# Kernel optimization log

Measured on AMD Instinct MI355X. Metric: run time of the kernel, lower is better.

The kernel has to match this reference:

```python
import jax, jax.numpy as jnp
import numpy as np

K = 4  # Chebyshev order (layer._k)

def setup_inputs() -> dict:
    key = jax.random.key(0)
    k1, k2, k3, k4 = jax.random.split(key, 4)
    N, din, dout = 4096, 128, 128
    a = jax.random.normal(k1, (N, din), dtype=jnp.float32)            # layer input (only len used)
    r = jax.random.uniform(k2, (N, dout), dtype=jnp.float32)          # upstream relevance (positive)
    # sparse-ish binary directed adjacency, no self loops (avg degree ~16)
    adj = (jax.random.uniform(k3, (N, N)) < (16.0 / N)).astype(jnp.float32)
    adj = adj * (1.0 - jnp.eye(N, dtype=jnp.float32))
    W = jax.random.normal(k4, (dout, K * din), dtype=jnp.float32) * 0.05  # ChebConv linear weight [out, K*in]
    return {"a": a, "r": r, "adj": adj, "W": W}

def _forward(a, r, adj, W):
    N = a.shape[0]
    dW = W.shape[1] // K
    # Wk[k] = W[:, k*dW:(k+1)*dW].T  -> [K, dimY(in), dimJ(out)]; rho = abs
    rhoW = jnp.abs(jnp.stack([W[:, k * dW:(k + 1) * dW].T for k in range(K)]))
    # Laplacian: L = I - D^{-1/2} A D^{-1/2}, degrees clamped at 1 (in-degrees = column sums)
    dinv = jnp.clip(adj.sum(axis=0), 1.0, None) ** -0.5
    D = dinv[:, None] * adj * dinv[None, :]
    L = jnp.eye(N, dtype=adj.dtype) - D
    # Chebyshev polynomials T_0=I, T_1=L, T_k = 2 L T_{k-1} - T_{k-2}  -> [K, N, N]
    Ts = [jnp.eye(N, dtype=L.dtype), L]
    for _ in range(2, K):
        Ts.append(2.0 * (L @ Ts[-1]) - Ts[-2])
    Ak = jnp.stack(Ts[:K])
    # U[i,j,x,y] = sum_k Ak[k,i,x] * rhoW[k,y,j]; never materialized.
    # denom[i,j] = U.sum(dim=(2,3)) = sum_k (sum_x Ak[k,i,x]) * (sum_y rhoW[k,y,j])
    denom = jnp.einsum('ki,kj->ij', Ak.sum(axis=2), rhoW.sum(axis=1))
    c = r / denom
    # out[x,y] = einsum('ijxy,ij->xy', U, c) = sum_k Ak[k].T @ c @ rhoW[k].T
    return jnp.einsum('kix,kyj,ij->xy', Ak, rhoW, c)

def reference(a, r, adj, W):
    return _forward(a, r, adj, W)
```

## Files before the change

### kernel.cpp

```cpp
#include <hip/hip_runtime.h>
#include <cstdint>
#include <cstddef>

#define N_NODES 4096
#define FEAT 128
#define KCH 4
#define NNZ_CAP (1 << 18)
#define TB 512
#define T2CAP 2048
#define RSTRIDE 96

__device__ __forceinline__ int panel_of(int p) {
    return p < 3456 ? (p / 384) : (p < 3776 ? 9 : 10);
}

__global__ __launch_bounds__(256) void k_adj(const float* __restrict__ adj,
                                             int* __restrict__ deg,
                                             int* __restrict__ rdeg,
                                             int* __restrict__ rcolF) {
    int row = (blockIdx.x * 256 + threadIdx.x) >> 6;
    int lane = threadIdx.x & 63;
    const float* rowp = adj + (size_t)row * N_NODES;
    int base = 0;
    for (int it = 0; it < 64; ++it) {
        int x = it * 64 + lane;
        bool nz = rowp[x] != 0.0f;
        unsigned long long m = __ballot(nz);
        if (nz) {
            int idx = base + __popcll(m & ((1ull << lane) - 1ull));
            if (idx < RSTRIDE) rcolF[row * RSTRIDE + idx] = x;
            atomicAdd(&deg[x], 1);
        }
        base += __popcll(m);
    }
    if (lane == 0) rdeg[row] = (base > RSTRIDE) ? RSTRIDE : base;
}

__global__ __launch_bounds__(1024) void k_scan(const int* __restrict__ deg,
                                               float* __restrict__ dinv,
                                               int* __restrict__ colptr,
                                               int* __restrict__ colcur) {
    __shared__ int wsum[16];
    __shared__ int wbase[16];
    int t = threadIdx.x;
    int lane = t & 63, wv = t >> 6;
    int v[4]; int s = 0;
    for (int c = 0; c < 4; ++c) {
        int idx = t * 4 + c;
        int di = deg[idx];
        v[c] = di;
        s += di;
        float dc = fmaxf((float)di, 1.0f);
        dinv[idx] = (float)(1.0 / sqrt((double)dc));
    }
    int sc = s;
    for (int off = 1; off < 64; off <<= 1) {
        int n = __shfl_up(sc, off);
        if (lane >= off) sc += n;
    }
    if (lane == 63) wsum[wv] = sc;
    __syncthreads();
    if (t == 0) {
        int b = 0;
        for (int q2 = 0; q2 < 16; ++q2) { wbase[q2] = b; b += wsum[q2]; }
    }
    __syncthreads();
    int base = wbase[wv] + sc - s;
    for (int c = 0; c < 4; ++c) {
        int idx = t * 4 + c;
        colptr[idx] = base; colcur[idx] = base;
        base += v[c];
    }
    if (t == 1023) colptr[N_NODES] = base;
}

__global__ __launch_bounds__(256) void k_vals(const float* __restrict__ dinv,
                                              const int* __restrict__ rdeg,
                                              const int* __restrict__ rcolF,
                                              float* __restrict__ rlvalF,
                                              int* __restrict__ colcur,
                                              int* __restrict__ col_i,
                                              float* __restrict__ val) {
    int row = (blockIdx.x * 256 + threadIdx.x) >> 6;
    int lane = threadIdx.x & 63;
    int n = rdeg[row];
    float di = dinv[row];
    for (int e = lane; e < n; e += 64) {
        int x = rcolF[row * RSTRIDE + e];
        float dv = di * dinv[x];
        rlvalF[row * RSTRIDE + e] = -dv;
        int ec = atomicAdd(&colcur[x], 1);
        if (ec < NNZ_CAP) { col_i[ec] = row; val[ec] = dv; }
    }
}

__global__ void k_sw(const float* __restrict__ W, float* __restrict__ sW) {
    int tid = blockIdx.x * blockDim.x + threadIdx.x;
    int k = tid >> 7, j = tid & 127;
    float s = 0.f;
    for (int y = 0; y < FEAT; ++y)
        s += fabsf(W[(size_t)j * (KCH * FEAT) + k * FEAT + y]);
    sW[k * FEAT + j] = s;
}

__device__ __forceinline__ float np_pairwise_4096(const float* __restrict__ row,
                                                  float* r256, float* leaf,
                                                  float* bc, int t) {
    if (t < 256) {
        int L = t >> 3, j = t & 7;
        const float* p = row + L * 128 + j;
        float a = p[0];
        #pragma unroll
        for (int q = 1; q < 16; ++q) a += p[8 * q];
        r256[t] = a;
    }
    __syncthreads();
    if (t < 32) {
        const float* rr = r256 + t * 8;
        leaf[t] = ((rr[0] + rr[1]) + (rr[2] + rr[3])) + ((rr[4] + rr[5]) + (rr[6] + rr[7]));
    }
    __syncthreads();
    if (t == 0) {
        float v[32];
        #pragma unroll
        for (int q = 0; q < 32; ++q) v[q] = leaf[q];
        #pragma unroll
        for (int w = 16; w >= 1; w >>= 1)
            #pragma unroll
            for (int q = 0; q < 16; ++q)
                if (q < w) v[q] = v[2 * q] + v[2 * q + 1];
        bc[0] = v[0];
    }
    __syncthreads();
    float res = bc[0];
    __syncthreads();
    return res;
}

__global__ __launch_bounds__(TB) void k_t2(const int* __restrict__ rdeg,
                                           const int* __restrict__ rcolF,
                                           const float* __restrict__ rlvalF,
                                           int2* __restrict__ t2sp,
                                           int* __restrict__ t2cnt,
                                           float* __restrict__ sA) {
    __shared__ float gp[N_NODES];
    __shared__ int   scol[2048];
    __shared__ float sval[2048];
    __shared__ int   pcol[64];
    __shared__ float pLip[64];
    __shared__ int   pbeg[64], plen[64], poff[65];
    __shared__ int   ssplit;
    __shared__ float r256[256], leaf[32], bc[1];
    __shared__ int   wtot[8], wbase[8];
    int t = threadIdx.x;
    int i = blockIdx.x;
    int rp = i * RSTRIDE;
    int ol = rdeg[i];
    int cnt = ol + 1;
    if (cnt > 64) cnt = 64;
    if (t == 0) ssplit = 0;
    __syncthreads();
    if (t < ol && rcolF[rp + t] < i) atomicAdd(&ssplit, 1);
    __syncthreads();
    int split = ssplit;
    if (t < cnt) {
        int col; float lip;
        if (t < split)       { col = rcolF[rp + t];     lip = rlvalF[rp + t]; }
        else if (t == split) { col = i;                 lip = 1.0f; }
        else                 { col = rcolF[rp + t - 1]; lip = rlvalF[rp + t - 1]; }
        pcol[t] = col; pLip[t] = lip;
        pbeg[t] = col * RSTRIDE;
        plen[t] = rdeg[col] + 1;
    }
    float4* gp4 = (float4*)gp;
    const float4 z4 = make_float4(0.f, 0.f, 0.f, 0.f);
    #pragma unroll
    for (int u = 0; u < 2; ++u) gp4[t + u * TB] = z4;
    __syncthreads();
    if (t == 0) {
        int o = 0;
        for (int q = 0; q < cnt; ++q) { poff[q] = o; o += plen[q]; }
        poff[cnt] = o;
    }
    __syncthreads();
    int E = poff[cnt]; if (E > 2048) E = 2048;
    for (int idx = t; idx < E; idx += TB) {
        int lo = 0, hi = cnt - 1;
        while (lo < hi) { int mid = (lo + hi + 1) >> 1; if (poff[mid] <= idx) lo = mid; else hi = mid - 1; }
        int e = idx - poff[lo];
        if (e == plen[lo] - 1) { scol[idx] = pcol[lo]; sval[idx] = 1.0f; }
        else                   { scol[idx] = rcolF[pbeg[lo] + e]; sval[idx] = rlvalF[pbeg[lo] + e]; }
    }
    __syncthreads();
    int q0 = split;
    for (int e = t; e < plen[q0]; e += TB) { int idx = poff[q0] + e; gp[scol[idx]] = sval[idx]; }
    __syncthreads();
    float s1 = np_pairwise_4096(gp, r256, leaf, bc, t);
    for (int e = t; e < plen[q0]; e += TB) gp[scol[poff[q0] + e]] = 0.0f;
    __syncthreads();
    float tot[8];
    #pragma unroll
    for (int u = 0; u < 8; ++u) tot[u] = 0.0f;
    int q = 0;
    while (q < cnt) {
        int pid = panel_of(pcol[q]);
        while (q < cnt && panel_of(pcol[q]) == pid) {
            float lv = pLip[q];
            int o = poff[q], Lq = plen[q];
            for (int e = t; e < Lq; e += TB) {
                int idx = o + e; int x = scol[idx];
                gp[x] = fmaf(lv, sval[idx], gp[x]);
            }
            __syncthreads();
            ++q;
        }
        #pragma unroll
        for (int u2 = 0; u2 < 2; ++u2) {
            int idx = t + u2 * TB;
            float4 b = gp4[idx];
            tot[4 * u2 + 0] = tot[4 * u2 + 0] + b.x;
            tot[4 * u2 + 1] = tot[4 * u2 + 1] + b.y;
            tot[4 * u2 + 2] = tot[4 * u2 + 2] + b.z;
            tot[4 * u2 + 3] = tot[4 * u2 + 3] + b.w;
            gp4[idx] = z4;
        }
        __syncthreads();
    }
    #pragma unroll
    for (int u2 = 0; u2 < 2; ++u2) {
        int xb = 4 * t + 2048 * u2;
        float4 v;
        v.x = 2.0f * tot[4 * u2 + 0] - (xb + 0 == i ? 1.0f : 0.0f);
        v.y = 2.0f * tot[4 * u2 + 1] - (xb + 1 == i ? 1.0f : 0.0f);
        v.z = 2.0f * tot[4 * u2 + 2] - (xb + 2 == i ? 1.0f : 0.0f);
        v.w = 2.0f * tot[4 * u2 + 3] - (xb + 3 == i ? 1.0f : 0.0f);
        gp4[t + u2 * TB] = v;
    }
    __syncthreads();
    float s2 = np_pairwise_4096(gp, r256, leaf, bc, t);
    float4 ea = gp4[2 * t], eb = gp4[2 * t + 1];
    float ev[8] = {ea.x, ea.y, ea.z, ea.w, eb.x, eb.y, eb.z, eb.w};
    int cl = 0;
    #pragma unroll
    for (int u = 0; u < 8; ++u) cl += (ev[u] != 0.0f);
    int lane = t & 63, wv = t >> 6;
    int sc = cl;
    for (int off = 1; off < 64; off <<= 1) {
        int n = __shfl_up(sc, off);
        if (lane >= off) sc += n;
    }
    if (lane == 63) wtot[wv] = sc;
    __syncthreads();
    if (t == 0) {
        int b = 0;
        for (int wq = 0; wq < 8; ++wq) { wbase[wq] = b; b += wtot[wq]; }
        t2cnt[i] = (b > T2CAP) ? T2CAP : b;
    }
    __syncthreads();
    int pos = wbase[wv] + sc - cl;
    int2* dst = t2sp + (size_t)i * T2CAP;
    #pragma unroll
    for (int u = 0; u < 8; ++u) {
        if (ev[u] != 0.0f) {
            if (pos < T2CAP) dst[pos] = make_int2(t * 8 + u, __float_as_int(ev[u]));
            ++pos;
        }
    }
    if (t == 0) {
        sA[0 * N_NODES + i] = 1.0f;
        sA[1 * N_NODES + i] = s1;
        sA[2 * N_NODES + i] = s2;
    }
}

__global__ __launch_bounds__(TB) void k_t3(const int* __restrict__ rdeg,
                                           const int* __restrict__ rcolF,
                                           const float* __restrict__ rlvalF,
                                           const int2* __restrict__ t2sp,
                                           const int* __restrict__ t2cnt,
                                           float* __restrict__ sA) {
    __shared__ float gp[N_NODES];
    __shared__ int   pcol[64];
    __shared__ float pLip[64];
    __shared__ int   pnn[64];
    __shared__ int   ssplit;
    __shared__ float r256[256], leaf[32], bc[1];
    int t = threadIdx.x;
    int i = blockIdx.x;
    int rp = i * RSTRIDE;
    int ol = rdeg[i];
    int cnt = ol + 1;
    if (cnt > 64) cnt = 64;
    if (t == 0) ssplit = 0;
    __syncthreads();
    if (t < ol && rcolF[rp + t] < i) atomicAdd(&ssplit, 1);
    __syncthreads();
    int split = ssplit;
    if (t < cnt) {
        int col; float lip;
        if (t < split)       { col = rcolF[rp + t];     lip = rlvalF[rp + t]; }
        else if (t == split) { col = i;                  lip = 1.0f; }
        else                 { col = rcolF[rp + t - 1];  lip = rlvalF[rp + t - 1]; }
        pcol[t] = col; pLip[t] = lip; pnn[t] = t2cnt[col];
    }
    float4* gp4 = (float4*)gp;
    const float4 z4 = make_float4(0.f, 0.f, 0.f, 0.f);
    #pragma unroll
    for (int u2 = 0; u2 < 2; ++u2) gp4[t + u2 * TB] = z4;
    __syncthreads();
    float tot[8];
    #pragma unroll
    for (int u = 0; u < 8; ++u) tot[u] = 0.0f;
    int2 enb[4] = {make_int2(0, 0), make_int2(0, 0), make_int2(0, 0), make_int2(0, 0)};
    int nn_next = pnn[0];
    {
        const int2* sp = t2sp + (size_t)pcol[0] * T2CAP;
        #pragma unroll
        for (int u = 0; u < 4; ++u) { int e = t + u * TB; if (e < nn_next) enb[u] = sp[e]; }
    }
    int q = 0;
    while (q < cnt) {
        int2 cur[4];
        int nn_c = nn_next;
        #pragma unroll
        for (int u = 0; u < 4; ++u) cur[u] = enb[u];
        if (q + 1 < cnt) {
            nn_next = pnn[q + 1];
            const int2* sp = t2sp + (size_t)pcol[q + 1] * T2CAP;
            #pragma unroll
            for (int u = 0; u < 4; ++u) { int e = t + u * TB; if (e < nn_next) enb[u] = sp[e]; }
        }
        float lv = pLip[q];
        #pragma unroll
        for (int u = 0; u < 4; ++u) {
            int e = t + u * TB;
            if (e < nn_c) gp[cur[u].x] = fmaf(lv, __int_as_float(cur[u].y), gp[cur[u].x]);
        }
        __syncthreads();
        ++q;
        if (q == cnt || panel_of(pcol[q]) != panel_of(pcol[q - 1])) {
            #pragma unroll
            for (int u2 = 0; u2 < 2; ++u2) {
                int idx = t + u2 * TB;
                float4 b = gp4[idx];
                tot[4 * u2 + 0] = tot[4 * u2 + 0] + b.x;
                tot[4 * u2 + 1] = tot[4 * u2 + 1] + b.y;
                tot[4 * u2 + 2] = tot[4 * u2 + 2] + b.z;
                tot[4 * u2 + 3] = tot[4 * u2 + 3] + b.w;
                gp4[idx] = z4;
            }
            __syncthreads();
        }
    }
    #pragma unroll
    for (int u2 = 0; u2 < 2; ++u2) {
        float4 v;
        v.x = 2.0f * tot[4 * u2 + 0];
        v.y = 2.0f * tot[4 * u2 + 1];
        v.z = 2.0f * tot[4 * u2 + 2];
        v.w = 2.0f * tot[4 * u2 + 3];
        gp4[t + u2 * TB] = v;
    }
    __syncthreads();
    for (int e = t; e < ol; e += TB) { int x = rcolF[rp + e]; gp[x] = gp[x] - rlvalF[rp + e]; }
    if (t == 0) gp[i] = gp[i] - 1.0f;
    __syncthreads();
    float s3 = np_pairwise_4096(gp, r256, leaf, bc, t);
    if (t == 0) sA[3 * N_NODES + i] = s3;
}

__global__ __launch_bounds__(256) void k_cm(const float* __restrict__ r,
                                            const float* __restrict__ sA,
                                            const float* __restrict__ sW,
                                            const float* __restrict__ W,
                                            float* __restrict__ M) {
#pragma clang fp contract(off)
    __shared__ float cl[16][FEAT];
    int k = blockIdx.y;
    int ib = blockIdx.x * 16;
    int tx = threadIdx.x;
    int y = tx & 127, half = tx >> 7;
    for (int m = tx; m < 16 * FEAT; m += 256) {
        int i = ib + (m >> 7), j = m & 127;
        float denom = 0.0f;
        #pragma unroll
        for (int k2 = 0; k2 < KCH; ++k2) {
            float p = sA[k2 * N_NODES + i] * sW[k2 * FEAT + j];
            denom = denom + p;
        }
        cl[m >> 7][m & 127] = r[(size_t)i * FEAT + j] / denom;
    }
    __syncthreads();
    float acc[8];
    #pragma unroll
    for (int u = 0; u < 8; ++u) acc[u] = 0.0f;
    for (int j = 0; j < FEAT; ++j) {
        float a = fabsf(W[(size_t)j * (KCH * FEAT) + k * FEAT + y]);
        #pragma unroll
        for (int u = 0; u < 8; ++u) acc[u] += a * cl[half * 8 + u][j];
    }
    #pragma unroll
    for (int u = 0; u < 8; ++u)
        M[(size_t)k * N_NODES * FEAT + (size_t)(ib + half * 8 + u) * FEAT + y] = acc[u];
}

__global__ void k_h1(const int* __restrict__ colptr, const int* __restrict__ col_i,
                     const float* __restrict__ val, const float* __restrict__ M,
                     float* __restrict__ B2) {
    int x = blockIdx.x * 2 + (threadIdx.x >> 7);
    int y = threadIdx.x & 127;
    const float* M2 = M + (size_t)2 * N_NODES * FEAT;
    const float* M3 = M + (size_t)3 * N_NODES * FEAT;
    int e0 = colptr[x], e1 = colptr[x + 1];
    if (e1 > NNZ_CAP) e1 = NNZ_CAP;
    float g = 0.0f;
    for (int e = e0; e < e1; ++e)
        g += val[e] * M3[(size_t)col_i[e] * FEAT + y];
    size_t o = (size_t)x * FEAT + y;
    B2[o] = 2.0f * M2[o] + 4.0f * (M3[o] - g);
}

__global__ void k_h2(const int* __restrict__ colptr, const int* __restrict__ col_i,
                     const float* __restrict__ val, const float* __restrict__ M,
                     const float* __restrict__ B2, float* __restrict__ B3) {
    int x = blockIdx.x * 2 + (threadIdx.x >> 7);
    int y = threadIdx.x & 127;
    const float* M1 = M + (size_t)N_NODES * FEAT;
    const float* M3 = M + (size_t)3 * N_NODES * FEAT;
    int e0 = colptr[x], e1 = colptr[x + 1];
    if (e1 > NNZ_CAP) e1 = NNZ_CAP;
    float g = 0.0f;
    for (int e = e0; e < e1; ++e)
        g += val[e] * B2[(size_t)col_i[e] * FEAT + y];
    size_t o = (size_t)x * FEAT + y;
    B3[o] = (M1[o] - 3.0f * M3[o]) + (B2[o] - g);
}

__global__ void k_h3(const int* __restrict__ colptr, const int* __restrict__ col_i,
                     const float* __restrict__ val, const float* __restrict__ M,
                     const float* __restrict__ B3, float* __restrict__ out) {
    int x = blockIdx.x * 2 + (threadIdx.x >> 7);
    int y = threadIdx.x & 127;
    const float* M0 = M;
    const float* M2 = M + (size_t)2 * N_NODES * FEAT;
    int e0 = colptr[x], e1 = colptr[x + 1];
    if (e1 > NNZ_CAP) e1 = NNZ_CAP;
    float g = 0.0f;
    for (int e = e0; e < e1; ++e)
        g += val[e] * B3[(size_t)col_i[e] * FEAT + y];
    size_t o = (size_t)x * FEAT + y;
    out[o] = (M0[o] - M2[o]) + (B3[o] - g);
}

extern "C" void kernel_launch(void* const* d_in, const int* in_sizes, int n_in,
                              void* d_out, int out_size, void* d_ws, size_t ws_size,
                              hipStream_t stream) {
    const float* r   = (const float*)d_in[1];
    const float* adj = (const float*)d_in[2];
    const float* W   = (const float*)d_in[3];
    float* out = (float*)d_out;

    char* w = (char*)d_ws;
    auto take = [&](size_t bytes) {
        char* p = w;
        w += (bytes + 255) & ~(size_t)255;
        return p;
    };
    int*   deg    = (int*)take((size_t)N_NODES * 4);
    int*   rdeg   = (int*)take((size_t)N_NODES * 4);
    float* dinv   = (float*)take((size_t)N_NODES * 4);
    int*   colcur = (int*)take((size_t)N_NODES * 4);
    int*   colptr = (int*)take((size_t)(N_NODES + 1) * 4);
    int*   col_i  = (int*)take((size_t)NNZ_CAP * 4);
    float* val    = (float*)take((size_t)NNZ_CAP * 4);
    int*   rcolF  = (int*)take((size_t)N_NODES * RSTRIDE * 4);
    float* rlvalF = (float*)take((size_t)N_NODES * RSTRIDE * 4);
    float* sW     = (float*)take((size_t)KCH * FEAT * 4);
    float* sA     = (float*)take((size_t)KCH * N_NODES * 4);
    float* M      = (float*)take((size_t)KCH * N_NODES * FEAT * 4);
    float* B2     = (float*)take((size_t)N_NODES * FEAT * 4);
    float* B3     = (float*)take((size_t)N_NODES * FEAT * 4);
    int*   t2cnt  = (int*)take((size_t)N_NODES * 4);
    int2*  t2sp   = (int2*)take((size_t)N_NODES * T2CAP * 8);

    hipMemsetAsync(deg, 0, (size_t)N_NODES * 4, stream);
    k_adj<<<N_NODES / 4, 256, 0, stream>>>(adj, deg, rdeg, rcolF);
    k_scan<<<1, 1024, 0, stream>>>(deg, dinv, colptr, colcur);
    k_vals<<<N_NODES / 4, 256, 0, stream>>>(dinv, rdeg, rcolF, rlvalF,
                                            colcur, col_i, val);
    k_sw<<<2, 256, 0, stream>>>(W, sW);
    k_t2<<<N_NODES, TB, 0, stream>>>(rdeg, rcolF, rlvalF, t2sp, t2cnt, sA);
    k_t3<<<N_NODES, TB, 0, stream>>>(rdeg, rcolF, rlvalF, t2sp, t2cnt, sA);
    k_cm<<<dim3(N_NODES / 16, KCH), 256, 0, stream>>>(r, sA, sW, W, M);
    k_h1<<<N_NODES / 2, 256, 0, stream>>>(colptr, col_i, val, M, B2);
    k_h2<<<N_NODES / 2, 256, 0, stream>>>(colptr, col_i, val, M, B2, B3);
    k_h3<<<N_NODES / 2, 256, 0, stream>>>(colptr, col_i, val, M, B3, out);
}
```

Baseline: 363.9 us.

## Shrink k_t3 blocks to 256 threads, drop register prefetch, fold k_sw into k_vals

k_t3 now runs 256-thread blocks. The software-pipelined register prefetch of the next T2 row is replaced by a simple strided loop over the current row, with 16 per-thread accumulators instead of 8. The goal is lower register pressure and more resident blocks per CU for the LDS-scatter loop, at the cost of losing the load/compute overlap. The small |W| column-sum kernel is also merged into k_vals as two extra blocks, which saves one kernel launch.

New measurement: 343.4 us. -5.6%, faster.

```diff
diff --git a/kernel.cpp b/kernel.cpp
--- a/kernel.cpp
+++ b/kernel.cpp
@@ -7,6 +7,7 @@
 #define KCH 4
 #define NNZ_CAP (1 << 18)
 #define TB 512
+#define TB3 256
 #define T2CAP 2048
 #define RSTRIDE 96
 
@@ -80,7 +81,18 @@
                                               float* __restrict__ rlvalF,
                                               int* __restrict__ colcur,
                                               int* __restrict__ col_i,
-                                              float* __restrict__ val) {
+                                              float* __restrict__ val,
+                                              const float* __restrict__ W,
+                                              float* __restrict__ sW) {
+    if (blockIdx.x >= N_NODES / 4) {
+        int tid = (blockIdx.x - N_NODES / 4) * 256 + threadIdx.x;
+        int k = tid >> 7, j = tid & 127;
+        float s = 0.f;
+        for (int y = 0; y < FEAT; ++y)
+            s += fabsf(W[(size_t)j * (KCH * FEAT) + k * FEAT + y]);
+        sW[k * FEAT + j] = s;
+        return;
+    }
     int row = (blockIdx.x * 256 + threadIdx.x) >> 6;
     int lane = threadIdx.x & 63;
     int n = rdeg[row];
@@ -92,15 +104,6 @@
         int ec = atomicAdd(&colcur[x], 1);
         if (ec < NNZ_CAP) { col_i[ec] = row; val[ec] = dv; }
     }
-}
-
-__global__ void k_sw(const float* __restrict__ W, float* __restrict__ sW) {
-    int tid = blockIdx.x * blockDim.x + threadIdx.x;
-    int k = tid >> 7, j = tid & 127;
-    float s = 0.f;
-    for (int y = 0; y < FEAT; ++y)
-        s += fabsf(W[(size_t)j * (KCH * FEAT) + k * FEAT + y]);
-    sW[k * FEAT + j] = s;
 }
 
 __device__ __forceinline__ float np_pairwise_4096(const float* __restrict__ row,
@@ -273,12 +276,12 @@
     }
 }
 
-__global__ __launch_bounds__(TB) void k_t3(const int* __restrict__ rdeg,
-                                           const int* __restrict__ rcolF,
-                                           const float* __restrict__ rlvalF,
-                                           const int2* __restrict__ t2sp,
-                                           const int* __restrict__ t2cnt,
-                                           float* __restrict__ sA) {
+__global__ __launch_bounds__(TB3) void k_t3(const int* __restrict__ rdeg,
+                                            const int* __restrict__ rcolF,
+                                            const float* __restrict__ rlvalF,
+                                            const int2* __restrict__ t2sp,
+                                            const int* __restrict__ t2cnt,
+                                            float* __restrict__ sA) {
     __shared__ float gp[N_NODES];
     __shared__ int   pcol[64];
     __shared__ float pLip[64];
@@ -306,42 +309,28 @@
     float4* gp4 = (float4*)gp;
     const float4 z4 = make_float4(0.f, 0.f, 0.f, 0.f);
     #pragma unroll
-    for (int u2 = 0; u2 < 2; ++u2) gp4[t + u2 * TB] = z4;
-    __syncthreads();
-    float tot[8];
-    #pragma unroll
-    for (int u = 0; u < 8; ++u) tot[u] = 0.0f;
-    int2 enb[4] = {make_int2(0, 0), make_int2(0, 0), make_int2(0, 0), make_int2(0, 0)};
-    int nn_next = pnn[0];
-    {
-        const int2* sp = t2sp + (size_t)pcol[0] * T2CAP;
-        #pragma unroll
-        for (int u = 0; u < 4; ++u) { int e = t + u * TB; if (e < nn_next) enb[u] = sp[e]; }
-    }
+    for (int u2 = 0; u2 < 4; ++u2) gp4[t + u2 * TB3] = z4;
+    __syncthreads();
+    float tot[16];
+    #pragma unroll
+    for (int u = 0; u < 16; ++u) tot[u] = 0.0f;
     int q = 0;
     while (q < cnt) {
-        int2 cur[4];
-        int nn_c = nn_next;
-        #pragma unroll
-        for (int u = 0; u < 4; ++u) cur[u] = enb[u];
-        if (q + 1 < cnt) {
-            nn_next = pnn[q + 1];
-            const int2* sp = t2sp + (size_t)pcol[q + 1] * T2CAP;
-            #pragma unroll
-            for (int u = 0; u < 4; ++u) { int e = t + u * TB; if (e < nn_next) enb[u] = sp[e]; }
-        }
-        float lv = pLip[q];
-        #pragma unroll
-        for (int u = 0; u < 4; ++u) {
-            int e = t + u * TB;
-            if (e < nn_c) gp[cur[u].x] = fmaf(lv, __int_as_float(cur[u].y), gp[cur[u].x]);
-        }
-        __syncthreads();
+        {
+            float lv = pLip[q];
+            int nn = pnn[q];
+            const int2* sp = t2sp + (size_t)pcol[q] * T2CAP;
+            for (int e = t; e < nn; e += TB3) {
+                int2 en = sp[e];
+                gp[en.x] = fmaf(lv, __int_as_float(en.y), gp[en.x]);
+            }
+            __syncthreads();
+        }
         ++q;
         if (q == cnt || panel_of(pcol[q]) != panel_of(pcol[q - 1])) {
             #pragma unroll
-            for (int u2 = 0; u2 < 2; ++u2) {
-                int idx = t + u2 * TB;
+            for (int u2 = 0; u2 < 4; ++u2) {
+                int idx = t + u2 * TB3;
                 float4 b = gp4[idx];
                 tot[4 * u2 + 0] = tot[4 * u2 + 0] + b.x;
                 tot[4 * u2 + 1] = tot[4 * u2 + 1] + b.y;
@@ -353,16 +342,16 @@
         }
     }
     #pragma unroll
-    for (int u2 = 0; u2 < 2; ++u2) {
+    for (int u2 = 0; u2 < 4; ++u2) {
         float4 v;
         v.x = 2.0f * tot[4 * u2 + 0];
         v.y = 2.0f * tot[4 * u2 + 1];
         v.z = 2.0f * tot[4 * u2 + 2];
         v.w = 2.0f * tot[4 * u2 + 3];
-        gp4[t + u2 * TB] = v;
-    }
-    __syncthreads();
-    for (int e = t; e < ol; e += TB) { int x = rcolF[rp + e]; gp[x] = gp[x] - rlvalF[rp + e]; }
+        gp4[t + u2 * TB3] = v;
+    }
+    __syncthreads();
+    for (int e = t; e < ol; e += TB3) { int x = rcolF[rp + e]; gp[x] = gp[x] - rlvalF[rp + e]; }
     if (t == 0) gp[i] = gp[i] - 1.0f;
     __syncthreads();
     float s3 = np_pairwise_4096(gp, r256, leaf, bc, t);
@@ -486,11 +475,10 @@
     hipMemsetAsync(deg, 0, (size_t)N_NODES * 4, stream);
     k_adj<<<N_NODES / 4, 256, 0, stream>>>(adj, deg, rdeg, rcolF);
     k_scan<<<1, 1024, 0, stream>>>(deg, dinv, colptr, colcur);
-    k_vals<<<N_NODES / 4, 256, 0, stream>>>(dinv, rdeg, rcolF, rlvalF,
-                                            colcur, col_i, val);
-    k_sw<<<2, 256, 0, stream>>>(W, sW);
+    k_vals<<<N_NODES / 4 + 2, 256, 0, stream>>>(dinv, rdeg, rcolF, rlvalF,
+                                                colcur, col_i, val, W, sW);
     k_t2<<<N_NODES, TB, 0, stream>>>(rdeg, rcolF, rlvalF, t2sp, t2cnt, sA);
-    k_t3<<<N_NODES, TB, 0, stream>>>(rdeg, rcolF, rlvalF, t2sp, t2cnt, sA);
+    k_t3<<<N_NODES, TB3, 0, stream>>>(rdeg, rcolF, rlvalF, t2sp, t2cnt, sA);
     k_cm<<<dim3(N_NODES / 16, KCH), 256, 0, stream>>>(r, sA, sW, W, M);
     k_h1<<<N_NODES / 2, 256, 0, stream>>>(colptr, col_i, val, M, B2);
     k_h2<<<N_NODES / 2, 256, 0, stream>>>(colptr, col_i, val, M, B2, B3);
```
